# Kernel optimization log

Hardware: AMD Instinct MI355X
Metric: run time of the kernel (lower is better)

The kernel has to match this reference:

```python
import jax, jax.numpy as jnp
import numpy as np

D_MODEL = 512
NUM_HEADS = 8
D_K = D_MODEL // NUM_HEADS
D_FF = 2048
VOCAB = 32000
PAD_IDX = 0
SEQ = 2048
BATCH = 8
N_REPEAT = 6
# source computes ((d_model/num_heads)**1)/2 = 32.0 (precedence bug), not sqrt(d_k)
SCORE_DIV = (D_MODEL / NUM_HEADS) / 2.0
LN_EPS = 1e-5


def setup_inputs() -> dict:
    key = jax.random.key(0)
    ks = jax.random.split(key, 16)
    s = lambda fan_in: 1.0 / np.sqrt(fan_in)
    inp = {
        "ids": jax.random.randint(ks[0], (BATCH, SEQ), 0, VOCAB, dtype=jnp.int64)
               if jax.config.jax_enable_x64 else
               jax.random.randint(ks[0], (BATCH, SEQ), 0, VOCAB, dtype=jnp.int32),
        "emb": jax.random.normal(ks[1], (VOCAB, D_MODEL), jnp.float32),
        "Wq": jax.random.normal(ks[2], (D_MODEL, D_K), jnp.float32) * s(D_MODEL),
        "bq": jnp.zeros((D_K,), jnp.float32),
        "Wk": jax.random.normal(ks[3], (D_MODEL, D_K), jnp.float32) * s(D_MODEL),
        "bk": jnp.zeros((D_K,), jnp.float32),
        "Wv": jax.random.normal(ks[4], (D_MODEL, D_K), jnp.float32) * s(D_MODEL),
        "bv": jnp.zeros((D_K,), jnp.float32),
        "Wo": jax.random.normal(ks[5], (D_MODEL, D_MODEL), jnp.float32) * s(D_MODEL),
        "bo": jnp.zeros((D_MODEL,), jnp.float32),
        "W1": jax.random.normal(ks[6], (D_MODEL, D_FF), jnp.float32) * s(D_MODEL),
        "b1": jnp.zeros((D_FF,), jnp.float32),
        "W2": jax.random.normal(ks[7], (D_FF, D_MODEL), jnp.float32) * s(D_FF),
        "b2": jnp.zeros((D_MODEL,), jnp.float32),
    }
    # padding_idx row is zero in torch's nn.Embedding
    inp["emb"] = inp["emb"].at[PAD_IDX].set(0.0)
    return inp


def positional_encoding(seq_len, d_model):
    pos = jnp.arange(seq_len, dtype=jnp.float32)[:, None]          # [S,1]
    even_i = jnp.arange(0, d_model, 2, dtype=jnp.float32)          # actual indices 0,2,4,...
    odd_i = jnp.arange(1, d_model, 2, dtype=jnp.float32)
    pe_even = jnp.sin(pos / jnp.power(10000.0, 2.0 * even_i / d_model))  # [S,D/2]
    pe_odd = jnp.cos(pos / jnp.power(10000.0, 2.0 * odd_i / d_model))    # [S,D/2]
    pe = jnp.stack([pe_even, pe_odd], axis=2).reshape(seq_len, d_model)  # interleave
    return pe[None]  # [1,S,D]


def whole_tensor_layernorm(x):
    # F.layer_norm(x, normalized_shape=x.shape): normalize over ALL elems, no affine
    m = jnp.mean(x)
    v = jnp.mean(jnp.square(x - m))
    return (x - m) * jax.lax.rsqrt(v + LN_EPS)


def encoder_forward(ids, emb, Wq, bq, Wk, bk, Wv, bv, Wo, bo, W1, b1, W2, b2):
    mask = (ids != PAD_IDX)[..., None].astype(emb.dtype)
    x = emb[ids] * mask + positional_encoding(ids.shape[1], D_MODEL)  # [B,S,D]
    for _ in range(N_REPEAT):  # same weights reused every repeat (as in source)
        # all heads use the SAME q/k/v Linear -> compute once, tile NUM_HEADS times
        q = jnp.einsum("bsd,dk->bsk", x, Wq) + bq   # [B,S,64]
        k = jnp.einsum("bsd,dk->bsk", x, Wk) + bk
        v = jnp.einsum("bsd,dk->bsk", x, Wv) + bv
        scores = jnp.einsum("bsk,btk->bst", q, k) / SCORE_DIV  # [B,S,S]
        attn = jax.nn.softmax(scores, axis=-1)
        head = jnp.einsum("bst,btk->bsk", attn, v)             # [B,S,64]
        concat = jnp.tile(head, (1, 1, NUM_HEADS))             # [B,S,512]
        mha = jnp.einsum("bsd,de->bse", concat, Wo) + bo
        x1 = whole_tensor_layernorm(mha + x)
        ff = jnp.einsum("bsd,df->bsf", jax.nn.relu(jnp.einsum("bsd,df->bsf", x1, W1) + b1), W2) + b2
        x = whole_tensor_layernorm(x1 + ff)
    return x


def reference(ids, emb, Wq, bq, Wk, bk, Wv, bv, Wo, bo, W1, b1, W2, b2):
    return encoder_forward(ids, emb, Wq, bq, Wk, bk, Wv, bv, Wo, bo, W1, b1, W2, b2)
```

## Files before the change

kernel.cpp:

```cpp
#include <hip/hip_runtime.h>
#include <math.h>

#define BB 8
#define SS 2048
#define DM 512
#define DK 64
#define DFF 2048
#define ROWS (BB*SS)
#define NTOT (ROWS*DM)
#define LN_EPS 1e-5
#define PAD_IDX 0

typedef __attribute__((ext_vector_type(8))) short short8;
typedef __attribute__((ext_vector_type(4))) short s16x4;
typedef __attribute__((ext_vector_type(4))) float f32x4;

__device__ __forceinline__ short f2b(float f) {
    unsigned u = __float_as_uint(f);
    unsigned r = (u + 0x7fffu + ((u >> 16) & 1u)) >> 16;
    return (short)r;
}
__device__ __forceinline__ float b2f(short s) {
    return __uint_as_float(((unsigned)(unsigned short)s) << 16);
}

__global__ __launch_bounds__(256) void embed_kernel(const int* __restrict__ ids,
                                                    const float* __restrict__ emb,
                                                    short* __restrict__ T1,
                                                    double* __restrict__ red) {
    int idx = blockIdx.x * 256 + threadIdx.x;
    if (idx < 24) red[idx] = 0.0;
    if (idx >= NTOT) return;
    int d   = idx & (DM - 1);
    int row = idx >> 9;
    int s   = row & (SS - 1);
    int id  = ids[row];
    float e = (id != PAD_IDX) ? emb[(size_t)id * DM + d] : 0.0f;
    float ex  = 2.0f * (float)d / 512.0f;
    float div = powf(10000.0f, ex);
    float arg = (float)s / div;
    float pe  = (d & 1) ? cosf(arg) : sinf(arg);
    T1[idx] = f2b(e + pe);
}

__global__ __launch_bounds__(256) void packqkvT_kernel(const float* __restrict__ Wq,
                                                       const float* __restrict__ Wk,
                                                       const float* __restrict__ Wv,
                                                       const float* __restrict__ bq,
                                                       const float* __restrict__ bk,
                                                       const float* __restrict__ bv,
                                                       short* __restrict__ WqkvT,
                                                       float* __restrict__ bqkv) {
    int i = blockIdx.x * 256 + threadIdx.x;
    if (i < 256 * 512) {
        int n = i >> 9, k = i & 511;
        float v = (n < 64)  ? Wq[k * 64 + n]
                : (n < 128) ? Wk[k * 64 + (n - 64)]
                : (n < 192) ? Wv[k * 64 + (n - 128)] : 0.0f;
        WqkvT[i] = f2b(v);
    }
    if (i < 256)
        bqkv[i] = (i < 64) ? bq[i] : (i < 128) ? bk[i - 64] : (i < 192) ? bv[i - 128] : 0.0f;
}

__global__ __launch_bounds__(256) void wosumT_kernel(const float* __restrict__ Wo,
                                                     short* __restrict__ WoST) {
    int i = blockIdx.x * 256 + threadIdx.x;
    if (i >= 512 * 64) return;
    int e = i >> 6, k = i & 63;
    float s = 0.f;
#pragma unroll
    for (int h = 0; h < 8; ++h) s += Wo[(size_t)(h * 64 + k) * 512 + e];
    WoST[i] = f2b(s);
}

__global__ __launch_bounds__(256) void transpose_b16(const float* __restrict__ in,
                                                     short* __restrict__ out,
                                                     int R, int C) {
    __shared__ float tile[32][33];
    int bx = blockIdx.x * 32;
    int by = blockIdx.y * 32;
    int tx = threadIdx.x & 31, ty = threadIdx.x >> 5;
#pragma unroll
    for (int i = 0; i < 32; i += 8)
        tile[ty + i][tx] = in[(size_t)(by + ty + i) * C + bx + tx];
    __syncthreads();
#pragma unroll
    for (int i = 0; i < 32; i += 8)
        out[(size_t)(bx + ty + i) * R + by + tx] = f2b(tile[tx][ty + i]);
}

__global__ __launch_bounds__(256) void colsum_kernel(const short* __restrict__ WqkvT,
                                                     const short* __restrict__ W1T,
                                                     float* __restrict__ csq,
                                                     float* __restrict__ csw1) {
    int i = blockIdx.x * 256 + threadIdx.x;
    if (i < 256) {
        const short* p = WqkvT + (size_t)i * 512;
        float s = 0.f;
        for (int k = 0; k < 512; ++k) s += b2f(p[k]);
        csq[i] = s;
    } else if (i < 2304) {
        int n = i - 256;
        const short* p = W1T + (size_t)n * 512;
        float s = 0.f;
        for (int k = 0; k < 512; ++k) s += b2f(p[k]);
        csw1[n] = s;
    }
}

__global__ __launch_bounds__(256) void vtrans_kernel(const short* __restrict__ qkvb,
                                                     short* __restrict__ Vtg) {
    __shared__ short tile[32][40];
    int sx = blockIdx.x * 32;
    int dy = blockIdx.y * 32;
    int b  = blockIdx.z;
    int tx = threadIdx.x & 31, ty = threadIdx.x >> 5;
#pragma unroll
    for (int i = 0; i < 32; i += 8)
        tile[ty + i][tx] = qkvb[(size_t)(b * SS + sx + ty + i) * 256 + 128 + dy + tx];
    __syncthreads();
#pragma unroll
    for (int i = 0; i < 32; i += 8)
        Vtg[(size_t)(b * 64 + dy + ty + i) * SS + sx + tx] = tile[tx][ty + i];
}

__device__ __forceinline__ void async16(const void* g, void* l) {
    __builtin_amdgcn_global_load_lds(
        (const __attribute__((address_space(1))) void*)g,
        (__attribute__((address_space(3))) void*)l, 16, 0, 0);
}

template <bool RELU, bool RESID, bool STATS, bool FOLD, int BM, int BN, int BK, int NBUF>
__global__ __launch_bounds__(256) void gemm_mfma(const short* __restrict__ A,
                                                 const short* __restrict__ BT,
                                                 const float* __restrict__ bias,
                                                 const float* __restrict__ colsum,
                                                 const short* __restrict__ residB,
                                                 short* __restrict__ C,
                                                 const double* __restrict__ statsIn,
                                                 double* __restrict__ statsOut,
                                                 int M, int N, int K) {
    constexpr int NT   = (BN == 256) ? 4 : ((BM == 128) ? 4 : 2);
    constexpr int KSUB = BK / 32;
    constexpr int RPS  = (BK == 32) ? 64 : 32;
    constexpr int LPS  = (BM + BN) / RPS;
    __shared__ short As[NBUF][BM * BK];
    __shared__ short Bs[NBUF][BN * BK];
    const int t   = threadIdx.x;
    const int wv  = t >> 6;
    const int l   = t & 63;
    const int q   = l >> 4,  l16 = l & 15;
    const int mbase = (BM == 128) ? (wv >> 1) * 64 : 0;
    const int nbase = (BM == 128) ? (wv & 1) * 64
                    : ((BN == 256) ? wv * 64 : wv * 32);
    const long m0 = (long)blockIdx.x * BM;
    const long n0 = (long)blockIdx.y * BN;

    float muf = 0.f, rstdf = 1.f;
    if (FOLD || RESID) {
        if (statsIn) {
            double mean = statsIn[0] * (1.0 / NTOT);
            double var  = statsIn[1] * (1.0 / NTOT) - mean * mean;
            muf   = (float)mean;
            rstdf = (float)(1.0 / sqrt(var + LN_EPS));
        }
    }

    f32x4 acc[4][NT] = {};

    const int srow = (BK == 32) ? (wv * 16 + (l >> 2)) : (wv * 8 + (l >> 3));
    const int kcol = (BK == 32) ? (((l & 3) ^ ((l >> 3) & 3)) * 8)
                                : (((l & 7) ^ ((l >> 3) & 7)) * 8);
    const int wrow = (BK == 32) ? wv * 16 : wv * 8;

    auto stage = [&](int buf, int k0) {
#pragma unroll
        for (int i = 0; i < BM / RPS; ++i)
            async16(A + (m0 + srow + i * RPS) * (long)K + k0 + kcol,
                    &As[buf][(wrow + i * RPS) * BK + l * 8]);
#pragma unroll
        for (int i = 0; i < BN / RPS; ++i)
            async16(BT + (n0 + srow + i * RPS) * (long)K + k0 + kcol,
                    &Bs[buf][(wrow + i * RPS) * BK + l * 8]);
    };
    auto waitcnt_steady = [&]() {
        if constexpr (LPS == 4)       asm volatile("s_waitcnt vmcnt(4)" ::: "memory");
        else if constexpr (LPS == 5)  asm volatile("s_waitcnt vmcnt(5)" ::: "memory");
        else if constexpr (LPS == 6)  asm volatile("s_waitcnt vmcnt(6)" ::: "memory");
        else                          asm volatile("s_waitcnt vmcnt(8)" ::: "memory");
    };

    stage(0, 0);
    if (K > BK) stage(1, BK);
    int cur = 0;
    for (int k0 = 0; k0 < K; k0 += BK) {
        if (k0 + BK < K) waitcnt_steady();
        else             asm volatile("s_waitcnt vmcnt(0)" ::: "memory");
        __builtin_amdgcn_sched_barrier(0);
        __builtin_amdgcn_s_barrier();
        __builtin_amdgcn_sched_barrier(0);

        short8 af[KSUB][4], bfr[KSUB][NT];
#pragma unroll
        for (int ks = 0; ks < KSUB; ++ks) {
            const int slot = (BK == 32) ? (q ^ ((l16 >> 1) & 3))
                                        : ((ks * 4 + q) ^ (l16 & 7));
#pragma unroll
            for (int i = 0; i < 4; ++i)
                af[ks][i] = *(const short8*)&As[cur][(mbase + i * 16 + l16) * BK + slot * 8];
#pragma unroll
            for (int i = 0; i < NT; ++i)
                bfr[ks][i] = *(const short8*)&Bs[cur][(nbase + i * 16 + l16) * BK + slot * 8];
        }

        if constexpr (NBUF == 2) {
            asm volatile("s_waitcnt lgkmcnt(0)" ::: "memory");
            __builtin_amdgcn_sched_barrier(0);
            __builtin_amdgcn_s_barrier();
            __builtin_amdgcn_sched_barrier(0);
            if (k0 + 2 * BK < K) stage(cur, k0 + 2 * BK);
        } else {
            if (k0 + 2 * BK < K) {
                int sb = cur + 2; if (sb >= 3) sb -= 3;
                stage(sb, k0 + 2 * BK);
            }
        }

        __builtin_amdgcn_s_setprio(1);
#pragma unroll
        for (int ks = 0; ks < KSUB; ++ks)
#pragma unroll
            for (int mt = 0; mt < 4; ++mt)
#pragma unroll
                for (int nt = 0; nt < NT; ++nt)
                    acc[mt][nt] = __builtin_amdgcn_mfma_f32_16x16x32_bf16(
                        af[ks][mt], bfr[ks][nt], acc[mt][nt], 0, 0, 0);
        __builtin_amdgcn_s_setprio(0);

        if constexpr (NBUF == 3) {
            asm volatile("s_waitcnt lgkmcnt(0)" ::: "memory");
            __builtin_amdgcn_sched_barrier(0);
        }

        cur += 1; if (cur >= NBUF) cur = 0;
    }

    const float mr = muf * rstdf;
    float s = 0.f, sq = 0.f;
#pragma unroll
    for (int mt = 0; mt < 4; ++mt) {
        const long rowb = m0 + mbase + mt * 16 + q * 4;
#pragma unroll
        for (int nt = 0; nt < NT; ++nt) {
            const long col = n0 + nbase + nt * 16 + l16;
            const float bv = bias[col];
            const float cs = FOLD ? colsum[col] : 0.f;
#pragma unroll
            for (int r = 0; r < 4; ++r) {
                const long idx = (rowb + r) * (long)N + col;
                float v = acc[mt][nt][r];
                if (FOLD) v = rstdf * v + bv - mr * cs;
                else      v = v + bv;
                if (RESID) v += (b2f(residB[idx]) - muf) * rstdf;
                if (RELU)  v = fmaxf(v, 0.0f);
                if (STATS) { s += v; sq += v * v; }
                C[idx] = f2b(v);
            }
        }
    }
    if (STATS) {
#pragma unroll
        for (int o = 32; o; o >>= 1) {
            s  += __shfl_down(s, o);
            sq += __shfl_down(sq, o);
        }
        __syncthreads();
        float* sm = (float*)As;
        if (l == 0) { sm[wv] = s; sm[4 + wv] = sq; }
        __syncthreads();
        if (t == 0) {
            atomicAdd(&statsOut[0], (double)(sm[0] + sm[1] + sm[2] + sm[3]));
            atomicAdd(&statsOut[1], (double)(sm[4] + sm[5] + sm[6] + sm[7]));
        }
    }
}

__global__ __launch_bounds__(256) void attn_mfma(const short* __restrict__ qkvb,
                                                 const short* __restrict__ Vtg,
                                                 short* __restrict__ head) {
    const int b  = blockIdx.y;
    const int q0 = blockIdx.x * 64;
    const int t  = threadIdx.x;
    const int w  = t >> 6;
    const int l  = t & 63;
    const int l15 = l & 15, lq = l >> 4;
    const int l7  = l & 7,  l8 = l >> 3;

    __shared__ short Ks[64][72];
    __shared__ short Vs[64][72];
    __shared__ short Ps[4][16][68];

    short8 qf[2];
    {
        const short* qrow = qkvb + (size_t)(b * SS + q0 + w * 16 + l15) * 256;
        qf[0] = *(const short8*)(qrow + lq * 8);
        qf[1] = *(const short8*)(qrow + 32 + lq * 8);
    }

    f32x4 acc[4];
#pragma unroll
    for (int mt = 0; mt < 4; ++mt) acc[mt] = {0.f, 0.f, 0.f, 0.f};
    float m_i = -INFINITY, l_i = 0.f;
    const float sc = 0.0450712500463f;

    short8 kreg[2], vreg[2];
    {
        const short* kb = qkvb + (size_t)(b * SS) * 256 + 64;
        kreg[0] = *(const short8*)(kb + (size_t)(w * 8 + l8) * 256 + l7 * 8);
        kreg[1] = *(const short8*)(kb + (size_t)(32 + w * 8 + l8) * 256 + l7 * 8);
        const short* vb = Vtg + (size_t)b * 64 * SS;
        vreg[0] = *(const short8*)(vb + (size_t)(w * 8 + l8) * SS + l7 * 8);
        vreg[1] = *(const short8*)(vb + (size_t)(32 + w * 8 + l8) * SS + l7 * 8);
    }

    for (int kt = 0; kt < SS / 64; ++kt) {
        __syncthreads();
        *(short8*)&Ks[w * 8 + l8][l7 * 8]      = kreg[0];
        *(short8*)&Ks[32 + w * 8 + l8][l7 * 8] = kreg[1];
        *(short8*)&Vs[w * 8 + l8][l7 * 8]      = vreg[0];
        *(short8*)&Vs[32 + w * 8 + l8][l7 * 8] = vreg[1];
        if (kt + 1 < SS / 64) {
            const short* kb = qkvb + (size_t)(b * SS + (kt + 1) * 64) * 256 + 64;
            kreg[0] = *(const short8*)(kb + (size_t)(w * 8 + l8) * 256 + l7 * 8);
            kreg[1] = *(const short8*)(kb + (size_t)(32 + w * 8 + l8) * 256 + l7 * 8);
            const short* vb = Vtg + (size_t)b * 64 * SS + (kt + 1) * 64;
            vreg[0] = *(const short8*)(vb + (size_t)(w * 8 + l8) * SS + l7 * 8);
            vreg[1] = *(const short8*)(vb + (size_t)(32 + w * 8 + l8) * SS + l7 * 8);
        }
        __syncthreads();

        f32x4 st[4];
#pragma unroll
        for (int mt = 0; mt < 4; ++mt) st[mt] = {0.f, 0.f, 0.f, 0.f};
#pragma unroll
        for (int kc = 0; kc < 2; ++kc)
#pragma unroll
            for (int mt = 0; mt < 4; ++mt) {
                short8 kf = *(const short8*)&Ks[mt * 16 + l15][kc * 32 + lq * 8];
                st[mt] = __builtin_amdgcn_mfma_f32_16x16x32_bf16(kf, qf[kc], st[mt], 0, 0, 0);
            }
        float mx = m_i;
#pragma unroll
        for (int mt = 0; mt < 4; ++mt)
#pragma unroll
            for (int r = 0; r < 4; ++r) {
                st[mt][r] *= sc;
                mx = fmaxf(mx, st[mt][r]);
            }
        mx = fmaxf(mx, __shfl_xor(mx, 16));
        mx = fmaxf(mx, __shfl_xor(mx, 32));
        float alpha = exp2f(m_i - mx);
        float rs = 0.f;
#pragma unroll
        for (int mt = 0; mt < 4; ++mt) {
            s16x4 pk;
#pragma unroll
            for (int r = 0; r < 4; ++r) {
                float p = exp2f(st[mt][r] - mx);
                rs += p;
                pk[r] = f2b(p);
            }
            *(s16x4*)&Ps[w][l15][mt * 16 + lq * 4] = pk;
        }
        rs += __shfl_xor(rs, 16);
        rs += __shfl_xor(rs, 32);
        l_i = l_i * alpha + rs;
        m_i = mx;
#pragma unroll
        for (int mt = 0; mt < 4; ++mt)
#pragma unroll
            for (int r = 0; r < 4; ++r) acc[mt][r] *= alpha;

#pragma unroll
        for (int kc = 0; kc < 2; ++kc) {
            s16x4 p0 = *(const s16x4*)&Ps[w][l15][kc * 32 + lq * 8];
            s16x4 p1 = *(const s16x4*)&Ps[w][l15][kc * 32 + lq * 8 + 4];
            short8 pf = __builtin_shufflevector(p0, p1, 0, 1, 2, 3, 4, 5, 6, 7);
#pragma unroll
            for (int mt = 0; mt < 4; ++mt) {
                short8 vf = *(const short8*)&Vs[mt * 16 + l15][kc * 32 + lq * 8];
                acc[mt] = __builtin_amdgcn_mfma_f32_16x16x32_bf16(vf, pf, acc[mt], 0, 0, 0);
            }
        }
    }
    float inv = 1.0f / l_i;
    short* out = head + (size_t)(b * SS + q0 + w * 16 + l15) * 64;
#pragma unroll
    for (int mt = 0; mt < 4; ++mt) {
        s16x4 o;
#pragma unroll
        for (int r = 0; r < 4; ++r) o[r] = f2b(acc[mt][r] * inv);
        *(s16x4*)&out[mt * 16 + lq * 4] = o;
    }
}

__global__ __launch_bounds__(256) void lnfinal_kernel(const short* __restrict__ y,
                                                      float* __restrict__ out,
                                                      const double* __restrict__ red,
                                                      int n) {
    double mean = red[0] / n;
    double var  = red[1] / n - mean * mean;
    float mu   = (float)mean;
    float rstd = (float)(1.0 / sqrt(var + LN_EPS));
    for (int i = blockIdx.x * blockDim.x + threadIdx.x; i < n;
         i += gridDim.x * blockDim.x)
        out[i] = (b2f(y[i]) - mu) * rstd;
}

extern "C" void kernel_launch(void* const* d_in, const int* in_sizes, int n_in,
                              void* d_out, int out_size, void* d_ws, size_t ws_size,
                              hipStream_t stream) {
    const int*   ids = (const int*)d_in[0];
    const float* emb = (const float*)d_in[1];
    const float* Wq  = (const float*)d_in[2];
    const float* bq  = (const float*)d_in[3];
    const float* Wk  = (const float*)d_in[4];
    const float* bk  = (const float*)d_in[5];
    const float* Wv  = (const float*)d_in[6];
    const float* bv  = (const float*)d_in[7];
    const float* Wo  = (const float*)d_in[8];
    const float* bo  = (const float*)d_in[9];
    const float* W1  = (const float*)d_in[10];
    const float* b1  = (const float*)d_in[11];
    const float* W2  = (const float*)d_in[12];
    const float* b2  = (const float*)d_in[13];

    float* xout = (float*)d_out;
    char* w = (char*)d_ws;

    const bool big = ws_size >= (size_t)105195712 + 256;

    short *qkvb, *Vtg, *head, *T1, *T2, *hch, *WqkvT, *WoST, *W1T, *W2T;
    float *bqkv, *csq, *csw1; double* red;

    if (big) {
        hch   = (short*)(w + 0);
        qkvb  = (short*)(w + 0);
        Vtg   = (short*)(w + 8388608);
        head  = (short*)(w + 10485760);
        T1    = (short*)(w + 67108864);
        T2    = (short*)(w + 83886080);
        WqkvT = (short*)(w + 100663296);
        bqkv  = (float*)(w + 100925440);
        csq   = (float*)(w + 100926464);
        WoST  = (short*)(w + 100927488);
        W1T   = (short*)(w + 100993024);
        csw1  = (float*)(w + 103090176);
        W2T   = (short*)(w + 103098368);
        red   = (double*)(w + 105195520);
    } else {
        hch   = (short*)(w + 0);
        qkvb  = (short*)(w + 0);
        Vtg   = (short*)(w + 8388608);
        head  = (short*)(w + 10485760);
        T1    = (short*)(w + 33554432);
        T2    = (short*)(w + 50331648);
        WqkvT = (short*)(w + 67108864);
        bqkv  = (float*)(w + 67371008);
        csq   = (float*)(w + 67372032);
        WoST  = (short*)(w + 67373056);
        W1T   = (short*)(w + 67438592);
        csw1  = (float*)(w + 69535744);
        W2T   = (short*)(w + 69543936);
        red   = (double*)(w + 71641088);
    }

    packqkvT_kernel<<<(256 * 512 + 255) / 256, 256, 0, stream>>>(Wq, Wk, Wv, bq, bk, bv, WqkvT, bqkv);
    wosumT_kernel<<<(512 * 64 + 255) / 256, 256, 0, stream>>>(Wo, WoST);
    transpose_b16<<<dim3(2048 / 32, 512 / 32), 256, 0, stream>>>(W1, W1T, 512, 2048);
    transpose_b16<<<dim3(512 / 32, 2048 / 32), 256, 0, stream>>>(W2, W2T, 2048, 512);
    colsum_kernel<<<9, 256, 0, stream>>>(WqkvT, W1T, csq, csw1);
    embed_kernel<<<NTOT / 256, 256, 0, stream>>>(ids, emb, T1, red);

    for (int rep = 0; rep < 6; ++rep) {
        const double* sprev = rep ? red + 4 * (rep - 1) + 2 : nullptr;
        double* red1 = red + 4 * rep;
        double* red2 = red + 4 * rep + 2;

        gemm_mfma<false, false, false, true, 64, 128, 64, 2><<<dim3(256, 2), 256, 0, stream>>>(
            T1, WqkvT, bqkv, csq, nullptr, qkvb, sprev, nullptr, ROWS, 256, DM);
        vtrans_kernel<<<dim3(SS / 32, 2, BB), 256, 0, stream>>>(qkvb, Vtg);
        attn_mfma<<<dim3(SS / 64, BB), 256, 0, stream>>>(qkvb, Vtg, head);
        gemm_mfma<false, true, true, false, 64, 128, 64, 2><<<dim3(256, 4), 256, 0, stream>>>(
            head, WoST, bo, nullptr, T1, T2, sprev, red1, ROWS, DM, DK);
        if (big) {
            gemm_mfma<true, false, false, true, 128, 128, 64, 2><<<dim3(128, 16), 256, 0, stream>>>(
                T2, W1T, b1, csw1, nullptr, hch, red1, nullptr, ROWS, DFF, DM);
            gemm_mfma<false, true, true, false, 64, 256, 32, 3><<<dim3(256, 2), 256, 0, stream>>>(
                hch, W2T, b2, nullptr, T2, T1, red1, red2, ROWS, DM, DFF);
        } else {
            for (int c = 0; c < 2; ++c) {
                const size_t off = (size_t)c * 8192 * DM;
                gemm_mfma<true, false, false, true, 128, 128, 64, 2><<<dim3(64, 16), 256, 0, stream>>>(
                    T2 + off, W1T, b1, csw1, nullptr, hch, red1, nullptr, 8192, DFF, DM);
                gemm_mfma<false, true, true, false, 64, 256, 32, 3><<<dim3(128, 2), 256, 0, stream>>>(
                    hch, W2T, b2, nullptr, T2 + off, T1 + off, red1, red2, 8192, DM, DFF);
            }
        }
    }
    lnfinal_kernel<<<4096, 256, 0, stream>>>(T1, xout, red + 4 * 5 + 2, NTOT);
}
```

Measured before the change: 1.323 ms.

## Add dedicated 256x256-tile FF1 GEMM kernel with 8 waves and phased pipelining

```diff
diff --git a/kernel.cpp b/kernel.cpp
--- a/kernel.cpp
+++ b/kernel.cpp
@@ -129,6 +129,134 @@
     __builtin_amdgcn_global_load_lds(
         (const __attribute__((address_space(1))) void*)g,
         (__attribute__((address_space(3))) void*)l, 16, 0, 0);
+}
+
+__global__ __launch_bounds__(512) void gemm_ff1_8p(const short* __restrict__ A,
+                                                   const short* __restrict__ BT,
+                                                   const float* __restrict__ bias,
+                                                   const float* __restrict__ colsum,
+                                                   short* __restrict__ C,
+                                                   const double* __restrict__ statsIn,
+                                                   int M, int N) {
+    constexpr int K = 512;
+    constexpr int NTILE = K / 64;
+    __shared__ short As[2][256 * 64];
+    __shared__ short Bs[2][256 * 64];
+    const int t   = threadIdx.x;
+    const int wid = t >> 6;
+    const int l   = t & 63;
+    const int q   = l >> 4, l16 = l & 15;
+    const int wm  = wid >> 2, wn = wid & 3;
+    const long m0 = (long)blockIdx.x * 256;
+    const long n0 = (long)blockIdx.y * 256;
+
+    float muf = 0.f, rstdf = 1.f;
+    if (statsIn) {
+        double mean = statsIn[0] * (1.0 / NTOT);
+        double var  = statsIn[1] * (1.0 / NTOT) - mean * mean;
+        muf   = (float)mean;
+        rstdf = (float)(1.0 / sqrt(var + LN_EPS));
+    }
+
+    f32x4 acc[8][4] = {};
+
+    const short* Ab = A  + m0 * K;
+    const short* Bb = BT + n0 * K;
+    const int srow = t >> 3;
+    const int kcol = ((t & 7) ^ ((t >> 3) & 7)) * 8;
+    const int rsl  = l16 & 7;
+
+    auto stageA = [&](int b, int T, int j) {
+        async16(Ab + (long)(j * 64 + srow) * K + T * 64 + kcol,
+                &As[b][j * 64 * 64 + t * 8]);
+    };
+    auto stageB = [&](int b, int T, int j) {
+        async16(Bb + (long)(j * 64 + srow) * K + T * 64 + kcol,
+                &Bs[b][j * 64 * 64 + t * 8]);
+    };
+
+#pragma unroll
+    for (int j = 0; j < 4; ++j) { stageA(0, 0, j); stageB(0, 0, j); }
+    asm volatile("s_waitcnt vmcnt(0)" ::: "memory");
+    __builtin_amdgcn_sched_barrier(0);
+    __builtin_amdgcn_s_barrier();
+    __builtin_amdgcn_sched_barrier(0);
+
+    short8 af[4][2];
+    for (int T = 0; T < NTILE; ++T) {
+        const int b = T & 1;
+#pragma unroll
+        for (int p = 0; p < 4; ++p) {
+            const int mq = p >> 1, nq = p & 1;
+            if (nq == 0) {
+#pragma unroll
+                for (int i = 0; i < 4; ++i)
+#pragma unroll
+                    for (int ks = 0; ks < 2; ++ks) {
+                        const int r  = wm * 128 + mq * 64 + i * 16 + l16;
+                        const int sl = (ks * 4 + q) ^ rsl;
+                        af[i][ks] = *(const short8*)&As[b][r * 64 + sl * 8];
+                    }
+            }
+            short8 bfr[2][2];
+#pragma unroll
+            for (int i = 0; i < 2; ++i)
+#pragma unroll
+                for (int ks = 0; ks < 2; ++ks) {
+                    const int r  = wn * 64 + nq * 32 + i * 16 + l16;
+                    const int sl = (ks * 4 + q) ^ rsl;
+                    bfr[i][ks] = *(const short8*)&Bs[b][r * 64 + sl * 8];
+                }
+            if (T + 1 < NTILE) {
+                if (p == 0) {
+#pragma unroll
+                    for (int j = 0; j < 4; ++j) stageA(b ^ 1, T + 1, j);
+                } else if (p == 1) {
+#pragma unroll
+                    for (int j = 0; j < 4; ++j) stageB(b ^ 1, T + 1, j);
+                }
+            }
+            __builtin_amdgcn_s_barrier();
+            asm volatile("s_waitcnt lgkmcnt(0)" ::: "memory");
+            __builtin_amdgcn_sched_barrier(0);
+            __builtin_amdgcn_s_setprio(1);
+#pragma unroll
+            for (int ks = 0; ks < 2; ++ks)
+#pragma unroll
+                for (int i = 0; i < 4; ++i)
+#pragma unroll
+                    for (int jn = 0; jn < 2; ++jn)
+                        acc[mq * 4 + i][nq * 2 + jn] =
+                            __builtin_amdgcn_mfma_f32_16x16x32_bf16(
+                                af[i][ks], bfr[jn][ks],
+                                acc[mq * 4 + i][nq * 2 + jn], 0, 0, 0);
+            __builtin_amdgcn_s_setprio(0);
+            if (p == 3 && T + 1 < NTILE) {
+                asm volatile("s_waitcnt vmcnt(0)" ::: "memory");
+                __builtin_amdgcn_sched_barrier(0);
+            }
+            __builtin_amdgcn_s_barrier();
+            __builtin_amdgcn_sched_barrier(0);
+        }
+    }
+
+    const float mr = muf * rstdf;
+#pragma unroll
+    for (int mt = 0; mt < 8; ++mt) {
+        const long rowb = m0 + wm * 128 + mt * 16 + q * 4;
+#pragma unroll
+        for (int nt = 0; nt < 4; ++nt) {
+            const long col = n0 + wn * 64 + nt * 16 + l16;
+            const float bv = bias[col];
+            const float cs = colsum[col];
+#pragma unroll
+            for (int r = 0; r < 4; ++r) {
+                float v = rstdf * acc[mt][nt][r] + bv - mr * cs;
+                v = fmaxf(v, 0.0f);
+                C[(rowb + r) * (long)N + col] = f2b(v);
+            }
+        }
+    }
 }
 
 template <bool RELU, bool RESID, bool STATS, bool FOLD, int BM, int BN, int BK, int NBUF>
@@ -185,7 +313,8 @@
                     &Bs[buf][(wrow + i * RPS) * BK + l * 8]);
     };
     auto waitcnt_steady = [&]() {
-        if constexpr (LPS == 4)       asm volatile("s_waitcnt vmcnt(4)" ::: "memory");
+        if constexpr (LPS == 3)       asm volatile("s_waitcnt vmcnt(3)" ::: "memory");
+        else if constexpr (LPS == 4)  asm volatile("s_waitcnt vmcnt(4)" ::: "memory");
         else if constexpr (LPS == 5)  asm volatile("s_waitcnt vmcnt(5)" ::: "memory");
         else if constexpr (LPS == 6)  asm volatile("s_waitcnt vmcnt(6)" ::: "memory");
         else                          asm volatile("s_waitcnt vmcnt(8)" ::: "memory");
@@ -495,15 +624,15 @@
         gemm_mfma<false, true, true, false, 64, 128, 64, 2><<<dim3(256, 4), 256, 0, stream>>>(
             head, WoST, bo, nullptr, T1, T2, sprev, red1, ROWS, DM, DK);
         if (big) {
-            gemm_mfma<true, false, false, true, 128, 128, 64, 2><<<dim3(128, 16), 256, 0, stream>>>(
-                T2, W1T, b1, csw1, nullptr, hch, red1, nullptr, ROWS, DFF, DM);
+            gemm_ff1_8p<<<dim3(64, 8), 512, 0, stream>>>(
+                T2, W1T, b1, csw1, hch, red1, ROWS, DFF);
             gemm_mfma<false, true, true, false, 64, 256, 32, 3><<<dim3(256, 2), 256, 0, stream>>>(
                 hch, W2T, b2, nullptr, T2, T1, red1, red2, ROWS, DM, DFF);
         } else {
             for (int c = 0; c < 2; ++c) {
                 const size_t off = (size_t)c * 8192 * DM;
-                gemm_mfma<true, false, false, true, 128, 128, 64, 2><<<dim3(64, 16), 256, 0, stream>>>(
-                    T2 + off, W1T, b1, csw1, nullptr, hch, red1, nullptr, 8192, DFF, DM);
+                gemm_ff1_8p<<<dim3(32, 8), 512, 0, stream>>>(
+                    T2 + off, W1T, b1, csw1, hch, red1, 8192, DFF);
                 gemm_mfma<false, true, true, false, 64, 256, 32, 3><<<dim3(128, 2), 256, 0, stream>>>(
                     hch, W2T, b2, nullptr, T2 + off, T1 + off, red1, red2, 8192, DM, DFF);
             }
```

After: 1.292 ms. -2.4%, faster.
